# Kernel tuning notes

Hardware: AMD Instinct MI355X
Metric: run time of the kernel (lower is better)

## Reference

```python
import jax, jax.numpy as jnp
import numpy as np

B, L, CIN, COUT, TEMB, N_MODES = 32, 8192, 64, 64, 256, 64
M = N_MODES // 2 + 1  # retained rfft modes = 33
EPS = 1e-5


def setup_inputs() -> dict:
    key = jax.random.key(0)
    ks = jax.random.split(key, 12)
    std_w = float(np.sqrt(1.0 / (2.0 * CIN)))
    # flax Dense default kernel init = lecun_normal ~ normal(std=1/sqrt(fan_in)); plain normal is fine for a reference
    return {
        "x": jax.random.normal(ks[0], (B, L, CIN), jnp.float32),
        "t_emb": jax.random.normal(ks[1], (B, TEMB), jnp.float32),
        # SpectralFreqTimeConv1D params
        "spec_w_real": jax.random.normal(ks[2], (M, CIN, COUT), jnp.float32) * std_w,
        "spec_w_imag": jax.random.normal(ks[3], (M, CIN, COUT), jnp.float32) * std_w,
        "dense_re": jax.random.normal(ks[4], (TEMB, M), jnp.float32) / np.sqrt(TEMB),
        "dense_im": jax.random.normal(ks[5], (TEMB, M), jnp.float32) / np.sqrt(TEMB),
        # TimeConv1D params
        "conv_kernel": jax.random.normal(ks[6], (CIN, COUT), jnp.float32) / np.sqrt(CIN),
        "conv_bias": jnp.zeros((COUT,), jnp.float32),
        "tc_weights": jax.random.normal(ks[7], (COUT, COUT), jnp.float32) * 0.01,  # nn.initializers.normal() stddev=0.01
        "psi_kernel": jax.random.normal(ks[8], (TEMB, 2 * COUT), jnp.float32) / np.sqrt(TEMB),
        # BatchNorm params
        "bn_scale": jnp.ones((COUT,), jnp.float32),
        "bn_bias": jnp.zeros((COUT,), jnp.float32),
    }


def reference(x, t_emb, spec_w_real, spec_w_imag, dense_re, dense_im,
              conv_kernel, conv_bias, tc_weights, psi_kernel, bn_scale, bn_bias):
    b, L_in, _ = x.shape
    n_freq = L_in // 2 + 1

    # ---- SpectralFreqTimeConv1D ----
    x_ft = jnp.fft.rfft(x, axis=-2, norm="forward")            # (b, n_freq, CIN) complex
    t_c = (t_emb @ dense_re) + 1j * (t_emb @ dense_im)         # (b, M) complex
    W = spec_w_real + 1j * spec_w_imag                          # (M, CIN, COUT) complex
    # diagonal-in-mode modulation: equivalent to the eye-based einsum chain
    out_m = t_c[:, :, None] * jnp.einsum("bmi,mio->bmo", x_ft[:, :M, :], W)  # (b, M, COUT)
    out_ft = jnp.zeros((b, n_freq, COUT), jnp.complex64).at[:, :M, :].set(out_m)
    x_spec = jnp.fft.irfft(out_ft, axis=-2, n=L_in, norm="forward")  # (b, L, COUT)

    # ---- TimeConv1D (residual branch) ----
    h = x @ conv_kernel + conv_bias                             # 1x1 conv: (b, L, COUT)
    psi = t_emb @ psi_kernel                                    # (b, 2*COUT)
    w_t, b_t = jnp.split(psi, 2, axis=-1)
    # einsum('ij,bjk,blk->bli', W, diag(w_t), h) == (h * w_t) @ W^T
    x_res = jnp.einsum("blj,ij->bli", h * w_t[:, None, :], tc_weights) + b_t[:, None, :]

    # ---- combine, batchnorm (training: batch stats), activation ----
    out = x_spec + x_res
    mean = out.mean(axis=(0, 1))
    var = out.var(axis=(0, 1))
    out = (out - mean) * jax.lax.rsqrt(var + EPS) * bn_scale + bn_bias
    return jax.nn.relu(out)
```

## Files before the change

### kernel.cpp

```cpp
#include <hip/hip_runtime.h>

typedef short short8 __attribute__((ext_vector_type(8)));
typedef float f32x4 __attribute__((ext_vector_type(4)));
typedef unsigned int u32;
typedef u32 u32x4 __attribute__((ext_vector_type(4)));
typedef unsigned short u16;

#define BB 32
#define LL 8192
#define TE 256
#define MM 33
#define INVL (1.0f/8192.0f)

#define TBLM_OFF 0
#define TTD_OFF  262144
#define VTB_OFF  589824
#define DD_OFF   720896
#define DD2_OFF  722944
#define BNP_OFF  731200

#define PART_OFF  0
#define SRED2_OFF 9437184
#define VF_OFF    9732096

static __device__ __forceinline__ u16 f2b(float f) {
  u32 u = __float_as_uint(f);
  return (u16)((u + 0x7FFFu + ((u >> 16) & 1u)) >> 16);
}
static __device__ __forceinline__ u32 pk2(float lo, float hi) {
  return __builtin_amdgcn_perm(__float_as_uint(hi) + 0x8000u,
                               __float_as_uint(lo) + 0x8000u,
                               0x07060302u);
}
static __device__ __forceinline__ float fsin(float rev) {
  float r; asm("v_sin_f32 %0, %1" : "=v"(r) : "v"(rev)); return r;
}
static __device__ __forceinline__ float fcos(float rev) {
  float r; asm("v_cos_f32 %0, %1" : "=v"(r) : "v"(rev)); return r;
}


__global__ __launch_bounds__(256) void k_tbl(float* __restrict__ ws) {
  u16* tb = (u16*)ws;
  u16* tt = (u16*)ws + TTD_OFF * 2;
  int bid = blockIdx.x, tid = threadIdx.x;
  if (bid < 1024) {
    int t = bid * 256 + tid;
    int l = t >> 5, m = (t & 31) + 1;
    float rev = (float)((m * l) & (LL - 1)) * INVL;
    int js = (m == 32) ? 0 : 32 + m;
    tb[l * 64 + m]  = f2b(fcos(rev));
    tb[l * 64 + js] = f2b(fsin(rev));
  } else if (bid < 2048) {
    int t = (bid - 1024) * 256 + tid;
    int m = (t >> 13) + 1, l = t & (LL - 1);
    float rev = (float)((m * l) & (LL - 1)) * INVL;
    int js = (m == 32) ? 0 : 32 + m;
    tt[m * LL + l]  = f2b(fcos(rev));
    tt[js * LL + l] = f2b(fsin(rev));
  } else {
    int t = (bid - 2048) * 256 + tid;
    int r = t >> 13;
    tt[(64 + r) * LL + (t & (LL - 1))] = (r == 0) ? 0x3F80u : 0u;
  }
}

__global__ __launch_bounds__(576) void k_dft(const float* __restrict__ x,
                                             const float* __restrict__ ws,
                                             float* __restrict__ scr) {
  __shared__ __align__(16) u16 sX[2][64 * 136];
  int tid = threadIdx.x;
  int b = blockIdx.x >> 5, chunk = blockIdx.x & 31;
  int l0 = chunk * 256;
  int w = tid >> 6, lane = tid & 63;
  const u16* tt = (const u16*)ws + TTD_OFF * 2;

  f32x4 acc[4];
#pragma unroll
  for (int ct = 0; ct < 4; ++ct) acc[ct] = (f32x4){0.f, 0.f, 0.f, 0.f};

  int arow = lane & 15;
  int kb = (lane >> 4) * 8;
  bool isg = (w >= 5);
  int gi = w - 5;
  bool stg = (tid < 512);
  int sc = tid & 63, lg = (tid >> 6) & 7;

  float vx[16];
  if (stg) {
#pragma unroll
    for (int i = 0; i < 16; ++i)
      vx[i] = x[(b * LL + l0 + lg * 16 + i) * 64 + sc];
    u32 wv[8];
#pragma unroll
    for (int j = 0; j < 8; ++j) wv[j] = pk2(vx[2 * j], vx[2 * j + 1]);
    u32x4* dst = (u32x4*)&sX[0][sc * 136 + lg * 16];
    dst[0] = (u32x4){wv[0], wv[1], wv[2], wv[3]};
    dst[1] = (u32x4){wv[4], wv[5], wv[6], wv[7]};
  }
  __syncthreads();

  if (stg) {
#pragma unroll
    for (int i = 0; i < 16; ++i)
      vx[i] = x[(b * LL + l0 + 128 + lg * 16 + i) * 64 + sc];
  }

#pragma unroll
  for (int kk = 0; kk < 4; ++kk) {
    short8 a = isg
      ? *reinterpret_cast<const short8*>(&sX[0][(gi * 16 + arow) * 136 + kk * 32 + kb])
      : *reinterpret_cast<const short8*>(tt + (w * 16 + arow) * LL + l0 + kk * 32 + kb);
#pragma unroll
    for (int ct = 0; ct < 4; ++ct) {
      short8 bf = *reinterpret_cast<const short8*>(&sX[0][(ct * 16 + arow) * 136 + kk * 32 + kb]);
      acc[ct] = __builtin_amdgcn_mfma_f32_16x16x32_bf16(a, bf, acc[ct], 0, 0, 0);
    }
  }

  if (stg) {
    u32 wv[8];
#pragma unroll
    for (int j = 0; j < 8; ++j) wv[j] = pk2(vx[2 * j], vx[2 * j + 1]);
    u32x4* dst = (u32x4*)&sX[1][sc * 136 + lg * 16];
    dst[0] = (u32x4){wv[0], wv[1], wv[2], wv[3]};
    dst[1] = (u32x4){wv[4], wv[5], wv[6], wv[7]};
  }
  __syncthreads();

#pragma unroll
  for (int kk = 0; kk < 4; ++kk) {
    short8 a = isg
      ? *reinterpret_cast<const short8*>(&sX[1][(gi * 16 + arow) * 136 + kk * 32 + kb])
      : *reinterpret_cast<const short8*>(tt + (w * 16 + arow) * LL + l0 + 128 + kk * 32 + kb);
#pragma unroll
    for (int ct = 0; ct < 4; ++ct) {
      short8 bf = *reinterpret_cast<const short8*>(&sX[1][(ct * 16 + arow) * 136 + kk * 32 + kb]);
      acc[ct] = __builtin_amdgcn_mfma_f32_16x16x32_bf16(a, bf, acc[ct], 0, 0, 0);
    }
  }

  int rowbase = isg ? (80 + gi * 16) : (w * 16);
  int rowb = (lane >> 4) * 4;
#pragma unroll
  for (int ct = 0; ct < 4; ++ct) {
    int col = ct * 16 + (lane & 15);
#pragma unroll
    for (int r = 0; r < 4; ++r)
      scr[PART_OFF + ((b * 32 + chunk) * 144 + rowbase + rowb + r) * 64 + col] = acc[ct][r];
  }
}

__global__ __launch_bounds__(256) void k_red1(float* __restrict__ scr) {
  int b = blockIdx.y;
  int r = blockIdx.x * 256 + threadIdx.x;
  float a = 0.f;
#pragma unroll 8
  for (int ch = 0; ch < 32; ++ch) a += scr[PART_OFF + (b * 32 + ch) * 9216 + r];
  scr[SRED2_OFF + b * 9216 + r] = a;
}

__global__ __launch_bounds__(256) void k_vb(
    const float* __restrict__ t_emb, const float* __restrict__ dre,
    const float* __restrict__ dim_, const float* __restrict__ pk,
    const float* __restrict__ swr, const float* __restrict__ swi,
    const float* __restrict__ ck, const float* __restrict__ cbias,
    const float* __restrict__ tw, float* __restrict__ scr,
    float* __restrict__ ws) {
  __shared__ float smem[12352];
  int tid = threadIdx.x;

  if (blockIdx.x < 33) {
    int m = blockIdx.x;
    float2* sW = (float2*)smem;
    float2* sX = (float2*)(smem + 8192);
    float* sTcb = smem + 8192 + 4096;

    for (int idx = tid; idx < 8192; idx += 256) smem[idx] = t_emb[idx];
    __syncthreads();
    if (tid < 64) {
      int b = tid & 31;
      const float* dd = (tid < 32) ? dre : dim_;
      float a = 0.f;
#pragma unroll 8
      for (int j = 0; j < TE; ++j) a = fmaf(smem[b * 256 + j], dd[j * MM + m], a);
      sTcb[tid] = a;
    }
    __syncthreads();

    for (int idx = tid; idx < 4096; idx += 256)
      sW[idx] = make_float2(swr[m * 4096 + idx], swi[m * 4096 + idx]);
    for (int idx = tid; idx < 2048; idx += 256) {
      int b = idx >> 6, i = idx & 63;
      const float* sr = scr + SRED2_OFF + b * 9216;
      float xr, xi;
      if (m == 0)      { xr = sr[64 * 64 + i] * INVL;  xi = 0.f; }
      else if (m < 32) { xr = sr[m * 64 + i] * INVL;   xi = -sr[(32 + m) * 64 + i] * INVL; }
      else             { xr = sr[32 * 64 + i] * INVL;  xi = -sr[0 * 64 + i] * INVL; }
      sX[idx] = make_float2(xr, xi);
    }
    __syncthreads();

    int w = tid >> 6, lane = tid & 63;
    for (int p = 0; p < 8; ++p) {
      int b = p * 4 + w;
      float a0 = 0.f, a1 = 0.f, a2 = 0.f, a3 = 0.f;
#pragma unroll 16
      for (int i = 0; i < 64; ++i) {
        float2 wv = sW[i * 64 + lane];
        float2 xv = sX[b * 64 + i];
        a0 = fmaf(xv.x, wv.x, a0);
        a1 = fmaf(xv.y, wv.y, a1);
        a2 = fmaf(xv.x, wv.y, a2);
        a3 = fmaf(xv.y, wv.x, a3);
      }
      float ar = a0 - a1, ai = a2 + a3;
      float tcr = sTcb[b], tci = sTcb[32 + b];
      float cr = tcr * ar - tci * ai;
      float ci = tcr * ai + tci * ar;
      if (m == 0) {
        ws[DD2_OFF + b * 64 + lane] = cr;
      } else {
        float crr = 2.f * cr, cii = -2.f * ci;
        int js = (m == 32) ? 0 : 32 + m;
        u16* vtb = (u16*)ws + VTB_OFF * 2 + (b * 64 + lane) * 128;
        vtb[64 + m] = f2b(crr);
        vtb[64 + js] = f2b(cii);
        float* vf = scr + VF_OFF + b * 8192;
        vf[(64 + m) * 64 + lane] = crr;
        vf[(64 + js) * 64 + lane] = cii;
      }
    }
  } else {
    int b = blockIdx.x - 33;
    float* sCkT = smem;
    float* sPtw = smem + 4096;
    float* sTe  = smem + 8192;
    float* sPsi = smem + 8448;

    sTe[tid] = t_emb[b * 256 + tid];
    __syncthreads();
    if (tid < 128) {
      float a = 0.f;
#pragma unroll 8
      for (int j = 0; j < TE; ++j) a = fmaf(sTe[j], pk[j * 128 + tid], a);
      sPsi[tid] = a;
    }
    __syncthreads();
    for (int idx = tid; idx < 4096; idx += 256) {
      int c = idx >> 6, j = idx & 63;
      sCkT[j * 64 + c] = ck[idx];
      sPtw[idx] = sPsi[j] * tw[idx];
    }
    __syncthreads();

    u16* vtb = (u16*)ws + VTB_OFF * 2 + b * 64 * 128;
    float* vf = scr + VF_OFF + b * 8192;
    int lane = tid & 63, w = tid >> 6;
#pragma unroll 4
    for (int it = 0; it < 16; ++it) {
      int o = it * 4 + w;
      float a = 0.f;
#pragma unroll 16
      for (int j = 0; j < 64; ++j)
        a = fmaf(sCkT[j * 64 + lane], sPtw[o * 64 + j], a);
      vtb[o * 128 + lane] = f2b(a);
      vf[lane * 64 + o] = a;
    }
    if (tid < 64) {
      float a = 0.f;
      for (int j = 0; j < 64; ++j) a = fmaf(cbias[j], sPtw[tid * 64 + j], a);
      ws[DD_OFF + b * 64 + tid] = a + sPsi[64 + tid];
    }
  }
}

__global__ __launch_bounds__(256) void k_bn(const float* __restrict__ scr,
                                            float* __restrict__ ws) {
  __shared__ float sVx[64 * 64];
  __shared__ float sGx[64 * 64];
  __shared__ float sS[64 * 64];
  __shared__ float sSum[64];
  __shared__ float sP[4][2][64];
  int tid = threadIdx.x, b = blockIdx.x;
  const float* sr = scr + SRED2_OFF + b * 9216;
  const float* vf = scr + VF_OFF + b * 8192;

  for (int p = tid; p < 4096; p += 256) {
    sVx[p] = vf[p];
    sGx[p] = sr[80 * 64 + p];
    sS[p]  = sr[p];
  }
  if (tid < 64) sSum[tid] = sr[64 * 64 + tid];
  __syncthreads();

  int o = tid & 63, part = tid >> 6;
  float m1 = 0.f, q1 = 0.f, cross = 0.f, vt2 = 0.f;
  for (int ii = 0; ii < 16; ++ii) {
    int i = part * 16 + ii;
    float vx = sVx[i * 64 + o];
    m1 = fmaf(sSum[i], vx, m1);
    float w0 = 0.f, w1 = 0.f, c0 = 0.f, c1 = 0.f;
#pragma unroll
    for (int j = 0; j < 64; j += 2) {
      float va = sVx[j * 64 + o], vb = sVx[(j + 1) * 64 + o];
      w0 = fmaf(sGx[i * 64 + j], va, w0);
      w1 = fmaf(sGx[i * 64 + j + 1], vb, w1);
      c0 = fmaf(sS[i * 64 + j], va, c0);
      c1 = fmaf(sS[i * 64 + j + 1], vb, c1);
    }
    q1 = fmaf(vx, w0 + w1, q1);
    float vt = vf[(64 + i) * 64 + o];
    vt2 = fmaf(vt, vt, vt2);
    cross = fmaf(vt, c0 + c1, cross);
  }
  sP[part][0][o] = m1;
  sP[part][1][o] = q1 + 2.f * cross + 4096.f * vt2;
  __syncthreads();
  if (tid < 64) {
    float m = sP[0][0][tid] + sP[1][0][tid] + sP[2][0][tid] + sP[3][0][tid];
    float q = sP[0][1][tid] + sP[1][1][tid] + sP[2][1][tid] + sP[3][1][tid];
    float D = ws[DD_OFF + b * 64 + tid] + ws[DD2_OFF + b * 64 + tid];
    ws[BNP_OFF + b * 128 + tid]      = m + 8192.f * D;
    ws[BNP_OFF + b * 128 + 64 + tid] = q + 2.f * D * m + 8192.f * D * D;
  }
}

__global__ __launch_bounds__(256) void k_main(const float* __restrict__ x,
                                              const float* __restrict__ ws,
                                              const float* __restrict__ bns,
                                              const float* __restrict__ bnb,
                                              float* __restrict__ out) {
  __shared__ __align__(16) u16 sVt[64 * 136];
  __shared__ float sD[64];
  __shared__ float sA[64];
  __shared__ float sB[64];
  __shared__ float sPp[4][64];
  __shared__ float sPq[4][64];
  int tid = threadIdx.x, w = tid >> 6, lane = tid & 63;
  int b = blockIdx.x >> 6, rg = blockIdx.x & 63;
  const u16* wsu = (const u16*)ws;

  {
    const u32* src = (const u32*)(wsu + VTB_OFF * 2 + b * 64 * 128);
    u32* dst = (u32*)sVt;
    for (int p = tid; p < 4096; p += 256)
      dst[(p >> 6) * 68 + (p & 63)] = src[p];
  }
  {
    int o = tid & 63, g = tid >> 6;
    float pm = 0.f, pq = 0.f;
#pragma unroll
    for (int r = 0; r < 8; ++r) {
      int bb = g * 8 + r;
      pm += ws[BNP_OFF + bb * 128 + o];
      pq += ws[BNP_OFF + bb * 128 + 64 + o];
    }
    sPp[g][o] = pm;
    sPq[g][o] = pq;
  }
  if (tid < 64) sD[tid] = ws[DD_OFF + b * 64 + tid] + ws[DD2_OFF + b * 64 + tid];
  __syncthreads();
  if (tid < 64) {
    const float inv_n = 1.f / (32.f * 8192.f);
    float mean = (sPp[0][tid] + sPp[1][tid] + sPp[2][tid] + sPp[3][tid]) * inv_n;
    float ex2  = (sPq[0][tid] + sPq[1][tid] + sPq[2][tid] + sPq[3][tid]) * inv_n;
    float var = ex2 - mean * mean;
    float istd = rsqrtf(var + 1e-5f);
    float al = istd * bns[tid];
    sA[tid] = al;
    sB[tid] = bnb[tid] - mean * al;
  }
  __syncthreads();

  int kb = (lane >> 4) * 8;
  short8 bf[4][4];
#pragma unroll
  for (int kk = 0; kk < 4; ++kk)
#pragma unroll
    for (int ct = 0; ct < 4; ++ct)
      bf[kk][ct] = *reinterpret_cast<const short8*>(
          &sVt[(ct * 16 + (lane & 15)) * 136 + kk * 32 + kb]);

  const u16* tb = wsu;
  int rowb = (lane >> 4) * 4;
  int lbase = rg * 128 + w * 32;

#pragma unroll
  for (int rt = 0; rt < 2; ++rt) {
    int l = lbase + rt * 16 + (lane & 15);
    const float* xq = x + (b * LL + l) * 64;
    float4 u0 = *reinterpret_cast<const float4*>(xq + kb);
    float4 u1 = *reinterpret_cast<const float4*>(xq + kb + 4);
    float4 u2 = *reinterpret_cast<const float4*>(xq + 32 + kb);
    float4 u3 = *reinterpret_cast<const float4*>(xq + 32 + kb + 4);
    union { short8 s; u32 wv[4]; } A0, A1;
    A0.wv[0] = pk2(u0.x, u0.y); A0.wv[1] = pk2(u0.z, u0.w);
    A0.wv[2] = pk2(u1.x, u1.y); A0.wv[3] = pk2(u1.z, u1.w);
    A1.wv[0] = pk2(u2.x, u2.y); A1.wv[1] = pk2(u2.z, u2.w);
    A1.wv[2] = pk2(u3.x, u3.y); A1.wv[3] = pk2(u3.z, u3.w);
    short8 a2 = *reinterpret_cast<const short8*>(tb + l * 64 + kb);
    short8 a3 = *reinterpret_cast<const short8*>(tb + l * 64 + 32 + kb);

    f32x4 acc[4];
#pragma unroll
    for (int ct = 0; ct < 4; ++ct) acc[ct] = (f32x4){0.f, 0.f, 0.f, 0.f};
#pragma unroll
    for (int ct = 0; ct < 4; ++ct) {
      acc[ct] = __builtin_amdgcn_mfma_f32_16x16x32_bf16(A0.s, bf[0][ct], acc[ct], 0, 0, 0);
      acc[ct] = __builtin_amdgcn_mfma_f32_16x16x32_bf16(A1.s, bf[1][ct], acc[ct], 0, 0, 0);
      acc[ct] = __builtin_amdgcn_mfma_f32_16x16x32_bf16(a2, bf[2][ct], acc[ct], 0, 0, 0);
      acc[ct] = __builtin_amdgcn_mfma_f32_16x16x32_bf16(a3, bf[3][ct], acc[ct], 0, 0, 0);
    }
#pragma unroll
    for (int ct = 0; ct < 4; ++ct) {
      int o = ct * 16 + (lane & 15);
      float dd = sD[o], al = sA[o], be = sB[o];
#pragma unroll
      for (int r = 0; r < 4; ++r) {
        float v = acc[ct][r] + dd;
        out[(b * LL + lbase + rt * 16 + rowb + r) * 64 + o] =
            fmaxf(fmaf(v, al, be), 0.f);
      }
    }
  }
}

extern "C" void kernel_launch(void* const* d_in, const int* in_sizes, int n_in,
                              void* d_out, int out_size, void* d_ws, size_t ws_size,
                              hipStream_t stream) {
  const float* x     = (const float*)d_in[0];
  const float* t_emb = (const float*)d_in[1];
  const float* swr   = (const float*)d_in[2];
  const float* swi   = (const float*)d_in[3];
  const float* dre   = (const float*)d_in[4];
  const float* dim_  = (const float*)d_in[5];
  const float* ck    = (const float*)d_in[6];
  const float* cbias = (const float*)d_in[7];
  const float* tw    = (const float*)d_in[8];
  const float* pk    = (const float*)d_in[9];
  const float* bns   = (const float*)d_in[10];
  const float* bnb   = (const float*)d_in[11];
  float* ws  = (float*)d_ws;
  float* out = (float*)d_out;

  k_tbl<<<2560, 256, 0, stream>>>(ws);
  k_dft<<<1024, 576, 0, stream>>>(x, ws, out);
  k_red1<<<dim3(36, 32), 256, 0, stream>>>(out);
  k_vb<<<65, 256, 0, stream>>>(t_emb, dre, dim_, pk, swr, swi,
                               ck, cbias, tw, out, ws);
  k_bn<<<32, 256, 0, stream>>>(out, ws);
  k_main<<<2048, 256, 0, stream>>>(x, ws, bns, bnb, out);
}
```

Baseline: 101.2 us.

## Store DFT partials as fp16 compactly and load main-kernel weights directly

The DFT kernel's per-chunk partial sums are now written as packed fp16 into a compact 129-row layout, with the unused padding rows dropped, instead of 144-row fp32. The reduction kernel reads half2 pairs and writes a smaller fp32 reduced buffer, and its launch grid is resized to match. This cuts the write and read traffic for the partials by more than half. Separately, k_main loads its bf16 B-fragments straight from global memory into registers, skipping the LDS staging pass and its shared buffer. fp16 partials add rounding error and overflow risk in the sums that feed the batch-norm statistics.

```diff
diff --git a/kernel.cpp b/kernel.cpp
--- a/kernel.cpp
+++ b/kernel.cpp
@@ -1,4 +1,5 @@
 #include <hip/hip_runtime.h>
+#include <hip/hip_fp16.h>
 
 typedef short short8 __attribute__((ext_vector_type(8)));
 typedef float f32x4 __attribute__((ext_vector_type(4)));
@@ -19,9 +20,8 @@
 #define DD2_OFF  722944
 #define BNP_OFF  731200
 
-#define PART_OFF  0
-#define SRED2_OFF 9437184
-#define VF_OFF    9732096
+#define SRED2_OFF 4227072
+#define VF_OFF    4491264
 
 static __device__ __forceinline__ u16 f2b(float f) {
   u32 u = __float_as_uint(f);
@@ -140,24 +140,36 @@
     }
   }
 
-  int rowbase = isg ? (80 + gi * 16) : (w * 16);
+  int rowbase = isg ? (65 + gi * 16) : (w * 16);
   int rowb = (lane >> 4) * 4;
+  u16* pp = (u16*)scr + (size_t)(b * 32 + chunk) * 129 * 64;
 #pragma unroll
   for (int ct = 0; ct < 4; ++ct) {
     int col = ct * 16 + (lane & 15);
 #pragma unroll
-    for (int r = 0; r < 4; ++r)
-      scr[PART_OFF + ((b * 32 + chunk) * 144 + rowbase + rowb + r) * 64 + col] = acc[ct][r];
+    for (int r = 0; r < 4; ++r) {
+      int sl = rowbase + rowb + r;
+      if (isg || sl < 65)
+        pp[sl * 64 + col] = __half_as_ushort(__float2half(acc[ct][r]));
+    }
   }
 }
 
 __global__ __launch_bounds__(256) void k_red1(float* __restrict__ scr) {
   int b = blockIdx.y;
-  int r = blockIdx.x * 256 + threadIdx.x;
-  float a = 0.f;
+  int p = blockIdx.x * 256 + threadIdx.x;
+  if (p >= 4128) return;
+  const u32* pb = (const u32*)scr + (size_t)b * 32 * 4128;
+  float a0 = 0.f, a1 = 0.f;
 #pragma unroll 8
-  for (int ch = 0; ch < 32; ++ch) a += scr[PART_OFF + (b * 32 + ch) * 9216 + r];
-  scr[SRED2_OFF + b * 9216 + r] = a;
+  for (int ch = 0; ch < 32; ++ch) {
+    u32 u = pb[ch * 4128 + p];
+    __half2 h2 = *reinterpret_cast<const __half2*>(&u);
+    float2 f = __half22float2(h2);
+    a0 += f.x; a1 += f.y;
+  }
+  *reinterpret_cast<float2*>(scr + SRED2_OFF + b * 8256 + 2 * p) =
+      make_float2(a0, a1);
 }
 
 __global__ __launch_bounds__(256) void k_vb(
@@ -192,7 +204,7 @@
       sW[idx] = make_float2(swr[m * 4096 + idx], swi[m * 4096 + idx]);
     for (int idx = tid; idx < 2048; idx += 256) {
       int b = idx >> 6, i = idx & 63;
-      const float* sr = scr + SRED2_OFF + b * 9216;
+      const float* sr = scr + SRED2_OFF + b * 8256;
       float xr, xi;
       if (m == 0)      { xr = sr[64 * 64 + i] * INVL;  xi = 0.f; }
       else if (m < 32) { xr = sr[m * 64 + i] * INVL;   xi = -sr[(32 + m) * 64 + i] * INVL; }
@@ -283,12 +295,12 @@
   __shared__ float sSum[64];
   __shared__ float sP[4][2][64];
   int tid = threadIdx.x, b = blockIdx.x;
-  const float* sr = scr + SRED2_OFF + b * 9216;
+  const float* sr = scr + SRED2_OFF + b * 8256;
   const float* vf = scr + VF_OFF + b * 8192;
 
   for (int p = tid; p < 4096; p += 256) {
     sVx[p] = vf[p];
-    sGx[p] = sr[80 * 64 + p];
+    sGx[p] = sr[65 * 64 + p];
     sS[p]  = sr[p];
   }
   if (tid < 64) sSum[tid] = sr[64 * 64 + tid];
@@ -331,7 +343,6 @@
                                               const float* __restrict__ bns,
                                               const float* __restrict__ bnb,
                                               float* __restrict__ out) {
-  __shared__ __align__(16) u16 sVt[64 * 136];
   __shared__ float sD[64];
   __shared__ float sA[64];
   __shared__ float sB[64];
@@ -341,12 +352,16 @@
   int b = blockIdx.x >> 6, rg = blockIdx.x & 63;
   const u16* wsu = (const u16*)ws;
 
-  {
-    const u32* src = (const u32*)(wsu + VTB_OFF * 2 + b * 64 * 128);
-    u32* dst = (u32*)sVt;
-    for (int p = tid; p < 4096; p += 256)
-      dst[(p >> 6) * 68 + (p & 63)] = src[p];
-  }
+  int kb = (lane >> 4) * 8;
+  const u16* vtb = wsu + VTB_OFF * 2 + b * 64 * 128;
+  short8 bf[4][4];
+#pragma unroll
+  for (int kk = 0; kk < 4; ++kk)
+#pragma unroll
+    for (int ct = 0; ct < 4; ++ct)
+      bf[kk][ct] = *reinterpret_cast<const short8*>(
+          vtb + (ct * 16 + (lane & 15)) * 128 + kk * 32 + kb);
+
   {
     int o = tid & 63, g = tid >> 6;
     float pm = 0.f, pq = 0.f;
@@ -372,15 +387,6 @@
     sB[tid] = bnb[tid] - mean * al;
   }
   __syncthreads();
-
-  int kb = (lane >> 4) * 8;
-  short8 bf[4][4];
-#pragma unroll
-  for (int kk = 0; kk < 4; ++kk)
-#pragma unroll
-    for (int ct = 0; ct < 4; ++ct)
-      bf[kk][ct] = *reinterpret_cast<const short8*>(
-          &sVt[(ct * 16 + (lane & 15)) * 136 + kk * 32 + kb]);
 
   const u16* tb = wsu;
   int rowb = (lane >> 4) * 4;
@@ -446,7 +452,7 @@
 
   k_tbl<<<2560, 256, 0, stream>>>(ws);
   k_dft<<<1024, 576, 0, stream>>>(x, ws, out);
-  k_red1<<<dim3(36, 32), 256, 0, stream>>>(out);
+  k_red1<<<dim3(17, 32), 256, 0, stream>>>(out);
   k_vb<<<65, 256, 0, stream>>>(t_emb, dre, dim_, pk, swr, swi,
                                ck, cbias, tw, out, ws);
   k_bn<<<32, 256, 0, stream>>>(out, ws);
```

Result: no change. 102.5 us (+1.3%).
